# Kernel tuning notes

Measured on AMD Instinct MI355X. Metric: run time of the kernel, lower is better.

Reference implementation:

```python
import jax, jax.numpy as jnp
import numpy as np

COST_BBOX = 1.0
COST_GIOU = 1.0
TOPK = 5


def _make_boxes(key, b, n):
    # valid xyxy boxes in [0,1]: centers + small positive sizes
    kc, ks = jax.random.split(key)
    cxy = jax.random.uniform(kc, (b, n, 2))
    wh = jax.random.uniform(ks, (b, n, 2)) * 0.2 + 0.01
    return jnp.concatenate([cxy - wh / 2, cxy + wh / 2], axis=-1)


def setup_inputs() -> dict:
    key = jax.random.key(0)
    k1, k2, k3, k4 = jax.random.split(key, 4)
    B, NP, NG = 8, 5000, 300
    return {
        "pred_box": _make_boxes(k1, B, NP),
        "pred_obj": jax.random.normal(k3, (B, NP), dtype=jnp.float32),
        "gt_box": _make_boxes(k2, B, NG),
        "gt_obj": jax.random.normal(k4, (B, NG), dtype=jnp.float32),
    }


def pairwise_giou(pb, gb):
    # pb: [B,N,4], gb: [B,M,4] in xyxy -> giou [B,N,M]
    area_p = (pb[..., 2] - pb[..., 0]) * (pb[..., 3] - pb[..., 1])  # [B,N]
    area_g = (gb[..., 2] - gb[..., 0]) * (gb[..., 3] - gb[..., 1])  # [B,M]
    lt = jnp.maximum(pb[:, :, None, :2], gb[:, None, :, :2])  # [B,N,M,2]
    rb = jnp.minimum(pb[:, :, None, 2:], gb[:, None, :, 2:])
    wh = jnp.clip(rb - lt, 0.0)
    inter = wh[..., 0] * wh[..., 1]                                  # [B,N,M]
    union = area_p[:, :, None] + area_g[:, None, :] - inter
    iou = inter / union
    # smallest enclosing box
    lt_e = jnp.minimum(pb[:, :, None, :2], gb[:, None, :, :2])
    rb_e = jnp.maximum(pb[:, :, None, 2:], gb[:, None, :, 2:])
    wh_e = jnp.clip(rb_e - lt_e, 0.0)
    area_e = wh_e[..., 0] * wh_e[..., 1]
    return iou - (area_e - union) / area_e


def cost_matrix(pred_box, gt_box):
    # L1 cdist: [B,N,M]
    cost_bbox = jnp.sum(jnp.abs(pred_box[:, :, None, :] - gt_box[:, None, :, :]), axis=-1)
    cost_giou = 1.0 - pairwise_giou(pred_box, gt_box)
    return COST_BBOX * cost_bbox + COST_GIOU * cost_giou


def reference(pred_box, pred_obj, gt_box, gt_obj):
    C = cost_matrix(pred_box, gt_box)            # [B, N_pred, N_gt]
    Ct = jnp.swapaxes(C, 1, 2)                   # [B, N_gt, N_pred]
    _, idx = jax.lax.top_k(-Ct, TOPK)            # smallest-cost preds per gt: [B, N_gt, TOPK]
    B, M, _ = idx.shape
    matched_pred = idx.reshape(B, M * TOPK).astype(jnp.int32)
    matched_gt = jnp.broadcast_to(jnp.repeat(jnp.arange(M, dtype=jnp.int32), TOPK)[None, :], (B, M * TOPK))
    return matched_pred, matched_gt
```

## Files before the change

### kernel.cpp

```cpp
#include <hip/hip_runtime.h>

#pragma clang fp contract(off)

typedef unsigned long long u64;

#define TOPK 5
#define WAVES 4

#define CE(x, y) do { const u64 _a = (x), _b = (y); const bool _l = _b < _a; \
                      (x) = _l ? _b : _a; (y) = _l ? _a : _b; } while (0)

#define INSERT(nk, k0, k1, k2, k3, k4) do {        \
    const u64 _n = (nk);                           \
    const bool l0 = _n < k0;                       \
    const bool l1 = _n < k1;                       \
    const bool l2 = _n < k2;                       \
    const bool l3 = _n < k3;                       \
    const bool l4 = _n < k4;                       \
    k4 = l4 ? (l3 ? k3 : _n) : k4;                 \
    k3 = l3 ? (l2 ? k2 : _n) : k3;                 \
    k2 = l2 ? (l1 ? k1 : _n) : k2;                 \
    k1 = l1 ? (l0 ? k0 : _n) : k1;                 \
    k0 = l0 ? _n : k0;                             \
} while (0)

__device__ __forceinline__ float fast_div(float a, float b) {
    float r = __builtin_amdgcn_rcpf(b);
    r = fmaf(fmaf(-b, r, 1.0f), r, r);
    float q = a * r;
    q = fmaf(fmaf(-b, q, a), r, q);
    return q;
}

__device__ __forceinline__ u64 eval_key(const float4 pb, const float4 gb,
                                        const float g_area, const int p) {
    const float area_p = (pb.z - pb.x) * (pb.w - pb.y);
    const float cost_bbox = fabsf(pb.x - gb.x) + fabsf(pb.y - gb.y)
                          + fabsf(pb.z - gb.z) + fabsf(pb.w - gb.w);
    const float ltx = fmaxf(pb.x, gb.x), lty = fmaxf(pb.y, gb.y);
    const float rbx = fminf(pb.z, gb.z), rby = fminf(pb.w, gb.w);
    const float iw = fmaxf(rbx - ltx, 0.0f), ih = fmaxf(rby - lty, 0.0f);
    const float inter = iw * ih;
    const float uni = area_p + g_area - inter;
    const float iou = fast_div(inter, uni);
    const float ex1 = fminf(pb.x, gb.x), ey1 = fminf(pb.y, gb.y);
    const float ex2 = fmaxf(pb.z, gb.z), ey2 = fmaxf(pb.w, gb.w);
    const float area_e = (ex2 - ex1) * (ey2 - ey1);
    const float giou = iou - fast_div(area_e - uni, area_e);
    const float cost = cost_bbox + (1.0f - giou);
    return ((u64)__float_as_uint(cost) << 32) | (unsigned)p;
}

__global__ __launch_bounds__(64 * WAVES) void matcher_topk_kernel(
    const float* __restrict__ pred_box,
    const float* __restrict__ gt_box,
    int* __restrict__ out_pred,
    int* __restrict__ out_gt,
    int B, int NP, int NG)
{
    const int task = blockIdx.x;
    const int wid  = threadIdx.x >> 6;
    const int lane = threadIdx.x & 63;
    const int b = task / NG;
    const int m = task - b * NG;

    const float4 gb = ((const float4*)gt_box)[b * NG + m];
    const float g_area = (gb.z - gb.x) * (gb.w - gb.y);

    u64 k0 = ~0ULL, k1 = ~0ULL, k2 = ~0ULL, k3 = ~0ULL, k4 = ~0ULL;

    const float4* pbase = (const float4*)pred_box + (size_t)b * NP;

    int p = threadIdx.x;
    for (; p + 256 < NP; p += 512) {
        const float4 pA = pbase[p];
        const float4 pB = pbase[p + 256];
        const u64 kA = eval_key(pA, gb, g_area, p);
        const u64 kB = eval_key(pB, gb, g_area, p + 256);
        INSERT(kA, k0, k1, k2, k3, k4);
        INSERT(kB, k0, k1, k2, k3, k4);
    }
    if (p < NP) {
        const float4 pA = pbase[p];
        const u64 kA = eval_key(pA, gb, g_area, p);
        INSERT(kA, k0, k1, k2, k3, k4);
    }

    #pragma unroll
    for (int off = 1; off < 64; off <<= 1) {
        const u64 b0 = __shfl_xor(k0, off);
        const u64 b1 = __shfl_xor(k1, off);
        const u64 b2 = __shfl_xor(k2, off);
        const u64 b3 = __shfl_xor(k3, off);
        const u64 b4 = __shfl_xor(k4, off);
        u64 m0 = k0 < b4 ? k0 : b4;
        u64 m1 = k1 < b3 ? k1 : b3;
        u64 m2 = k2 < b2 ? k2 : b2;
        u64 m3 = k3 < b1 ? k3 : b1;
        u64 m4 = k4 < b0 ? k4 : b0;
        CE(m0, m1); CE(m3, m4); CE(m2, m4); CE(m2, m3); CE(m1, m4);
        CE(m0, m3); CE(m0, m2); CE(m1, m3); CE(m1, m2);
        k0 = m0; k1 = m1; k2 = m2; k3 = m3; k4 = m4;
    }

    __shared__ u64 lds[WAVES][TOPK];
    if (lane == 0) {
        lds[wid][0] = k0; lds[wid][1] = k1; lds[wid][2] = k2;
        lds[wid][3] = k3; lds[wid][4] = k4;
    }
    __syncthreads();

    if (threadIdx.x == 0) {
        int head[WAVES];
        #pragma unroll
        for (int w = 0; w < WAVES; ++w) head[w] = 0;
        const int base = task * TOPK;
        #pragma unroll
        for (int r = 0; r < TOPK; ++r) {
            u64 best = ~0ULL; int bw = 0;
            #pragma unroll
            for (int w = 0; w < WAVES; ++w) {
                const u64 v = lds[w][head[w]];
                if (v < best) { best = v; bw = w; }
            }
            head[bw]++;
            out_pred[base + r] = (int)(unsigned)(best & 0xFFFFFFFFu);
            out_gt[base + r]   = m;
        }
    }
}

extern "C" void kernel_launch(void* const* d_in, const int* in_sizes, int n_in,
                              void* d_out, int out_size, void* d_ws, size_t ws_size,
                              hipStream_t stream) {
    const float* pred_box = (const float*)d_in[0];
    const float* gt_box   = (const float*)d_in[2];

    const int NP = 5000;
    const int B  = in_sizes[1] / NP;
    const int NG = in_sizes[3] / B;

    int* out_pred = (int*)d_out;
    int* out_gt   = out_pred + B * NG * TOPK;

    const int total = B * NG;
    hipLaunchKernelGGL(matcher_topk_kernel, dim3(total), dim3(64 * WAVES), 0, stream,
                       pred_box, gt_box, out_pred, out_gt, B, NP, NG);
}
```

Before: 42.01 us.

## Prune candidates by L1 lower bound and split blocks across two GTs

```diff
diff --git a/kernel.cpp b/kernel.cpp
--- a/kernel.cpp
+++ b/kernel.cpp
@@ -32,11 +32,10 @@
     return q;
 }
 
-__device__ __forceinline__ u64 eval_key(const float4 pb, const float4 gb,
-                                        const float g_area, const int p) {
+__device__ __forceinline__ u64 eval_rest(const float4 pb, const float cb,
+                                         const float4 gb, const float g_area,
+                                         const int p) {
     const float area_p = (pb.z - pb.x) * (pb.w - pb.y);
-    const float cost_bbox = fabsf(pb.x - gb.x) + fabsf(pb.y - gb.y)
-                          + fabsf(pb.z - gb.z) + fabsf(pb.w - gb.w);
     const float ltx = fmaxf(pb.x, gb.x), lty = fmaxf(pb.y, gb.y);
     const float rbx = fminf(pb.z, gb.z), rby = fminf(pb.w, gb.w);
     const float iw = fmaxf(rbx - ltx, 0.0f), ih = fmaxf(rby - lty, 0.0f);
@@ -47,7 +46,7 @@
     const float ex2 = fmaxf(pb.z, gb.z), ey2 = fmaxf(pb.w, gb.w);
     const float area_e = (ex2 - ex1) * (ey2 - ey1);
     const float giou = iou - fast_div(area_e - uni, area_e);
-    const float cost = cost_bbox + (1.0f - giou);
+    const float cost = cb + (1.0f - giou);
     return ((u64)__float_as_uint(cost) << 32) | (unsigned)p;
 }
 
@@ -58,33 +57,80 @@
     int* __restrict__ out_gt,
     int B, int NP, int NG)
 {
-    const int task = blockIdx.x;
+    const int pairsPerB = (NG + 1) >> 1;
+    const int tp = blockIdx.x;
+    const int b  = tp / pairsPerB;
+    const int j  = tp - b * pairsPerB;
+    const int m0 = 2 * j;
+    const bool has1 = (m0 + 1 < NG);
+
     const int wid  = threadIdx.x >> 6;
     const int lane = threadIdx.x & 63;
-    const int b = task / NG;
-    const int m = task - b * NG;
+    const int myGt = wid >> 1;
+    const int half = wid & 1;
 
-    const float4 gb = ((const float4*)gt_box)[b * NG + m];
+    const int m = m0 + (has1 ? myGt : 0);
+    const float4 gb = ((const float4*)gt_box)[b * NG + (myGt ? (has1 ? m0 + 1 : m0) : m0)];
     const float g_area = (gb.z - gb.x) * (gb.w - gb.y);
 
+    const int NPm1 = NP - 1;
+    const int hN   = (NP + 1) >> 1;
+    const int start = half ? hN : 0;
+    const int pend  = half ? NP : hN;
+    int niter = (pend - start + 255) >> 8;
+    niter += (niter & 1);
+
     u64 k0 = ~0ULL, k1 = ~0ULL, k2 = ~0ULL, k3 = ~0ULL, k4 = ~0ULL;
+    unsigned thr_u = 0xFFFFFFFFu;
 
     const float4* pbase = (const float4*)pred_box + (size_t)b * NP;
 
-    int p = threadIdx.x;
-    for (; p + 256 < NP; p += 512) {
-        const float4 pA = pbase[p];
-        const float4 pB = pbase[p + 256];
-        const u64 kA = eval_key(pA, gb, g_area, p);
-        const u64 kB = eval_key(pB, gb, g_area, p + 256);
-        INSERT(kA, k0, k1, k2, k3, k4);
-        INSERT(kB, k0, k1, k2, k3, k4);
+#define LOADG(it, ra, rb, rc, rd) do {                        \
+    const int _i = start + (it) * 256 + lane;                 \
+    ra = pbase[min(_i,       NPm1)];                          \
+    rb = pbase[min(_i + 64,  NPm1)];                          \
+    rc = pbase[min(_i + 128, NPm1)];                          \
+    rd = pbase[min(_i + 192, NPm1)];                          \
+} while (0)
+
+#define PROC1(pb_, idx_) do {                                            \
+    const float _cb = fabsf(pb_.x - gb.x) + fabsf(pb_.y - gb.y)          \
+                    + fabsf(pb_.z - gb.z) + fabsf(pb_.w - gb.w);         \
+    const bool _valid = (idx_) < pend;                                   \
+    const bool _want = (__float_as_uint(_cb) < thr_u) && _valid;         \
+    if (__any((int)_want)) {                                             \
+        u64 _k = eval_rest(pb_, _cb, gb, g_area, (idx_));                \
+        _k = _valid ? _k : ~0ULL;                                        \
+        INSERT(_k, k0, k1, k2, k3, k4);                                  \
+        thr_u = (unsigned)(k4 >> 32);                                    \
+    }                                                                    \
+} while (0)
+
+#define PROCG(it, ra, rb, rc, rd) do {                        \
+    const int _i0 = start + (it) * 256 + lane;                \
+    PROC1(ra, _i0);                                           \
+    PROC1(rb, _i0 + 64);                                      \
+    PROC1(rc, _i0 + 128);                                     \
+    PROC1(rd, _i0 + 192);                                     \
+} while (0)
+
+    float4 eA, eB, eC, eD;
+    float4 oA, oB, oC, oD;
+    LOADG(0, eA, eB, eC, eD);
+    LOADG(1, oA, oB, oC, oD);
+
+    const int nOuter = niter >> 1;
+    for (int k = 0; k < nOuter; ++k) {
+        const int itE = 2 * k;
+        PROCG(itE, eA, eB, eC, eD);
+        if (k + 1 < nOuter) LOADG(itE + 2, eA, eB, eC, eD);
+        PROCG(itE + 1, oA, oB, oC, oD);
+        if (k + 1 < nOuter) LOADG(itE + 3, oA, oB, oC, oD);
     }
-    if (p < NP) {
-        const float4 pA = pbase[p];
-        const u64 kA = eval_key(pA, gb, g_area, p);
-        INSERT(kA, k0, k1, k2, k3, k4);
-    }
+
+#undef LOADG
+#undef PROC1
+#undef PROCG
 
     #pragma unroll
     for (int off = 1; off < 64; off <<= 1) {
@@ -93,14 +139,14 @@
         const u64 b2 = __shfl_xor(k2, off);
         const u64 b3 = __shfl_xor(k3, off);
         const u64 b4 = __shfl_xor(k4, off);
-        u64 m0 = k0 < b4 ? k0 : b4;
-        u64 m1 = k1 < b3 ? k1 : b3;
-        u64 m2 = k2 < b2 ? k2 : b2;
-        u64 m3 = k3 < b1 ? k3 : b1;
-        u64 m4 = k4 < b0 ? k4 : b0;
-        CE(m0, m1); CE(m3, m4); CE(m2, m4); CE(m2, m3); CE(m1, m4);
-        CE(m0, m3); CE(m0, m2); CE(m1, m3); CE(m1, m2);
-        k0 = m0; k1 = m1; k2 = m2; k3 = m3; k4 = m4;
+        u64 m0_ = k0 < b4 ? k0 : b4;
+        u64 m1_ = k1 < b3 ? k1 : b3;
+        u64 m2_ = k2 < b2 ? k2 : b2;
+        u64 m3_ = k3 < b1 ? k3 : b1;
+        u64 m4_ = k4 < b0 ? k4 : b0;
+        CE(m0_, m1_); CE(m3_, m4_); CE(m2_, m4_); CE(m2_, m3_); CE(m1_, m4_);
+        CE(m0_, m3_); CE(m0_, m2_); CE(m1_, m3_); CE(m1_, m2_);
+        k0 = m0_; k1 = m1_; k2 = m2_; k3 = m3_; k4 = m4_;
     }
 
     __shared__ u64 lds[WAVES][TOPK];
@@ -110,22 +156,22 @@
     }
     __syncthreads();
 
-    if (threadIdx.x == 0) {
-        int head[WAVES];
-        #pragma unroll
-        for (int w = 0; w < WAVES; ++w) head[w] = 0;
-        const int base = task * TOPK;
-        #pragma unroll
-        for (int r = 0; r < TOPK; ++r) {
-            u64 best = ~0ULL; int bw = 0;
+    if (threadIdx.x < 2) {
+        const int which = threadIdx.x;
+        if (which == 0 || has1) {
+            const int mm = m0 + which;
+            int h0 = 0, h1 = 0;
+            const int base = (b * NG + mm) * TOPK;
             #pragma unroll
-            for (int w = 0; w < WAVES; ++w) {
-                const u64 v = lds[w][head[w]];
-                if (v < best) { best = v; bw = w; }
+            for (int r = 0; r < TOPK; ++r) {
+                const u64 v0 = lds[which * 2][h0];
+                const u64 v1 = lds[which * 2 + 1][h1];
+                const bool t = v0 < v1;
+                const u64 best = t ? v0 : v1;
+                h0 += t; h1 += !t;
+                out_pred[base + r] = (int)(unsigned)(best & 0xFFFFFFFFu);
+                out_gt[base + r]   = mm;
             }
-            head[bw]++;
-            out_pred[base + r] = (int)(unsigned)(best & 0xFFFFFFFFu);
-            out_gt[base + r]   = m;
         }
     }
 }
@@ -143,7 +189,8 @@
     int* out_pred = (int*)d_out;
     int* out_gt   = out_pred + B * NG * TOPK;
 
-    const int total = B * NG;
-    hipLaunchKernelGGL(matcher_topk_kernel, dim3(total), dim3(64 * WAVES), 0, stream,
+    const int pairsPerB = (NG + 1) >> 1;
+    const int blocks = B * pairsPerB;
+    hipLaunchKernelGGL(matcher_topk_kernel, dim3(blocks), dim3(64 * WAVES), 0, stream,
                        pred_box, gt_box, out_pred, out_gt, B, NP, NG);
 }
```

Result: faster. 38.74 us (-7.8%).

## Prune GIoU evaluation with an L1 lower bound and stage boxes in LDS

Applied to the files above, without the earlier changes.

```diff
diff --git a/kernel.cpp b/kernel.cpp
--- a/kernel.cpp
+++ b/kernel.cpp
@@ -6,6 +6,7 @@
 
 #define TOPK 5
 #define WAVES 4
+#define CHUNK 1024
 
 #define CE(x, y) do { const u64 _a = (x), _b = (y); const bool _l = _b < _a; \
                       (x) = _l ? _b : _a; (y) = _l ? _a : _b; } while (0)
@@ -32,11 +33,10 @@
     return q;
 }
 
-__device__ __forceinline__ u64 eval_key(const float4 pb, const float4 gb,
-                                        const float g_area, const int p) {
+__device__ __forceinline__ u64 eval_rest(const float4 pb, const float cb,
+                                         const float4 gb, const float g_area,
+                                         const int p) {
     const float area_p = (pb.z - pb.x) * (pb.w - pb.y);
-    const float cost_bbox = fabsf(pb.x - gb.x) + fabsf(pb.y - gb.y)
-                          + fabsf(pb.z - gb.z) + fabsf(pb.w - gb.w);
     const float ltx = fmaxf(pb.x, gb.x), lty = fmaxf(pb.y, gb.y);
     const float rbx = fminf(pb.z, gb.z), rby = fminf(pb.w, gb.w);
     const float iw = fmaxf(rbx - ltx, 0.0f), ih = fmaxf(rby - lty, 0.0f);
@@ -47,11 +47,11 @@
     const float ex2 = fmaxf(pb.z, gb.z), ey2 = fmaxf(pb.w, gb.w);
     const float area_e = (ex2 - ex1) * (ey2 - ey1);
     const float giou = iou - fast_div(area_e - uni, area_e);
-    const float cost = cost_bbox + (1.0f - giou);
+    const float cost = cb + (1.0f - giou);
     return ((u64)__float_as_uint(cost) << 32) | (unsigned)p;
 }
 
-__global__ __launch_bounds__(64 * WAVES) void matcher_topk_kernel(
+__global__ __launch_bounds__(256) void matcher_topk_kernel(
     const float* __restrict__ pred_box,
     const float* __restrict__ gt_box,
     int* __restrict__ out_pred,
@@ -59,32 +59,85 @@
     int B, int NP, int NG)
 {
     const int task = blockIdx.x;
-    const int wid  = threadIdx.x >> 6;
-    const int lane = threadIdx.x & 63;
+    const int t    = threadIdx.x;
+    const int wid  = t >> 6;
+    const int lane = t & 63;
     const int b = task / NG;
     const int m = task - b * NG;
 
     const float4 gb = ((const float4*)gt_box)[b * NG + m];
     const float g_area = (gb.z - gb.x) * (gb.w - gb.y);
 
+    __shared__ float4 sbuf[2][CHUNK];
+    __shared__ u64 smerge[WAVES][TOPK];
+
+    const float4* pbase = (const float4*)pred_box + (size_t)b * NP;
+    const int NPm1  = NP - 1;
+    const int NITER = (NP + CHUNK - 1) / CHUNK;
+
     u64 k0 = ~0ULL, k1 = ~0ULL, k2 = ~0ULL, k3 = ~0ULL, k4 = ~0ULL;
-
-    const float4* pbase = (const float4*)pred_box + (size_t)b * NP;
-
-    int p = threadIdx.x;
-    for (; p + 256 < NP; p += 512) {
-        const float4 pA = pbase[p];
-        const float4 pB = pbase[p + 256];
-        const u64 kA = eval_key(pA, gb, g_area, p);
-        const u64 kB = eval_key(pB, gb, g_area, p + 256);
-        INSERT(kA, k0, k1, k2, k3, k4);
-        INSERT(kB, k0, k1, k2, k3, k4);
-    }
-    if (p < NP) {
-        const float4 pA = pbase[p];
-        const u64 kA = eval_key(pA, gb, g_area, p);
-        INSERT(kA, k0, k1, k2, k3, k4);
-    }
+    unsigned thr_u = 0xFFFFFFFFu;
+
+    {
+        float4 r0 = pbase[min(t,       NPm1)];
+        float4 r1 = pbase[min(t + 256, NPm1)];
+        float4 r2 = pbase[min(t + 512, NPm1)];
+        float4 r3 = pbase[min(t + 768, NPm1)];
+        sbuf[0][t]       = r0;
+        sbuf[0][t + 256] = r1;
+        sbuf[0][t + 512] = r2;
+        sbuf[0][t + 768] = r3;
+    }
+    __syncthreads();
+
+#define PROC1(pb_, idx_) do {                                            \
+    const float _cb = fabsf(pb_.x - gb.x) + fabsf(pb_.y - gb.y)          \
+                    + fabsf(pb_.z - gb.z) + fabsf(pb_.w - gb.w);         \
+    const bool _valid = (idx_) < NP;                                     \
+    const bool _want = (__float_as_uint(_cb) < thr_u) && _valid;         \
+    if (__any((int)_want)) {                                             \
+        u64 _k = eval_rest(pb_, _cb, gb, g_area, (idx_));                \
+        _k = _valid ? _k : ~0ULL;                                        \
+        INSERT(_k, k0, k1, k2, k3, k4);                                  \
+        thr_u = (unsigned)(k4 >> 32);                                    \
+    }                                                                    \
+} while (0)
+
+    int cur = 0;
+    for (int it = 0; it < NITER; ++it) {
+        float4 r0, r1, r2, r3;
+        const bool more = (it + 1 < NITER);
+        if (more) {
+            const int nb = (it + 1) * CHUNK + t;
+            r0 = pbase[min(nb,       NPm1)];
+            r1 = pbase[min(nb + 256, NPm1)];
+            r2 = pbase[min(nb + 512, NPm1)];
+            r3 = pbase[min(nb + 768, NPm1)];
+        }
+        asm volatile("" ::: "memory");
+
+        const int base = it * CHUNK + t;
+        {
+            const float4 p0 = sbuf[cur][t];
+            PROC1(p0, base);
+            const float4 p1 = sbuf[cur][t + 256];
+            PROC1(p1, base + 256);
+            const float4 p2 = sbuf[cur][t + 512];
+            PROC1(p2, base + 512);
+            const float4 p3 = sbuf[cur][t + 768];
+            PROC1(p3, base + 768);
+        }
+
+        if (more) {
+            sbuf[cur ^ 1][t]       = r0;
+            sbuf[cur ^ 1][t + 256] = r1;
+            sbuf[cur ^ 1][t + 512] = r2;
+            sbuf[cur ^ 1][t + 768] = r3;
+            cur ^= 1;
+        }
+        __syncthreads();
+    }
+#undef PROC1
 
     #pragma unroll
     for (int off = 1; off < 64; off <<= 1) {
@@ -103,29 +156,28 @@
         k0 = m0; k1 = m1; k2 = m2; k3 = m3; k4 = m4;
     }
 
-    __shared__ u64 lds[WAVES][TOPK];
     if (lane == 0) {
-        lds[wid][0] = k0; lds[wid][1] = k1; lds[wid][2] = k2;
-        lds[wid][3] = k3; lds[wid][4] = k4;
+        smerge[wid][0] = k0; smerge[wid][1] = k1; smerge[wid][2] = k2;
+        smerge[wid][3] = k3; smerge[wid][4] = k4;
     }
     __syncthreads();
 
-    if (threadIdx.x == 0) {
+    if (t == 0) {
         int head[WAVES];
         #pragma unroll
         for (int w = 0; w < WAVES; ++w) head[w] = 0;
-        const int base = task * TOPK;
+        const int baseo = task * TOPK;
         #pragma unroll
         for (int r = 0; r < TOPK; ++r) {
             u64 best = ~0ULL; int bw = 0;
             #pragma unroll
             for (int w = 0; w < WAVES; ++w) {
-                const u64 v = lds[w][head[w]];
+                const u64 v = smerge[w][head[w]];
                 if (v < best) { best = v; bw = w; }
             }
             head[bw]++;
-            out_pred[base + r] = (int)(unsigned)(best & 0xFFFFFFFFu);
-            out_gt[base + r]   = m;
+            out_pred[baseo + r] = (int)(unsigned)(best & 0xFFFFFFFFu);
+            out_gt[baseo + r]   = m;
         }
     }
 }
@@ -144,6 +196,6 @@
     int* out_gt   = out_pred + B * NG * TOPK;
 
     const int total = B * NG;
-    hipLaunchKernelGGL(matcher_topk_kernel, dim3(total), dim3(64 * WAVES), 0, stream,
+    hipLaunchKernelGGL(matcher_topk_kernel, dim3(total), dim3(256), 0, stream,
                        pred_box, gt_box, out_pred, out_gt, B, NP, NG);
 }
```

Result: slower. 44.73 us (+6.5%).
